# Kernel tuning notes

Measured on AMD Instinct MI355X. Metric: run time of the kernel, lower is better.

The kernel has to match this reference:

```python
import jax, jax.numpy as jnp
import numpy as np

D_MODEL = 1024
N_HEADS = 16
HEAD_DIM = D_MODEL // N_HEADS


def setup_inputs() -> dict:
    key = jax.random.key(0)
    ks = jax.random.split(key, 5)
    x = jax.random.normal(ks[0], (2, 2048, D_MODEL), dtype=jnp.float32)
    s = 1.0 / np.sqrt(D_MODEL)
    W_qkv = jax.random.normal(ks[1], (D_MODEL, 3 * D_MODEL), dtype=jnp.float32) * s
    b_qkv = jnp.zeros((3 * D_MODEL,), dtype=jnp.float32)
    W_proj = jax.random.normal(ks[2], (D_MODEL, D_MODEL), dtype=jnp.float32) * s
    b_proj = jnp.zeros((D_MODEL,), dtype=jnp.float32)
    return {"x": x, "W_qkv": W_qkv, "b_qkv": b_qkv, "W_proj": W_proj, "b_proj": b_proj}


def reference(x, W_qkv, b_qkv, W_proj, b_proj):
    b, t, c = x.shape
    qkv = x @ W_qkv + b_qkv  # [b,t,3c]
    q, k, v = jnp.split(qkv, 3, axis=-1)
    # [b, h, t, d]
    q = q.reshape(b, t, N_HEADS, HEAD_DIM).transpose(0, 2, 1, 3)
    k = k.reshape(b, t, N_HEADS, HEAD_DIM).transpose(0, 2, 1, 3)
    v = v.reshape(b, t, N_HEADS, HEAD_DIM).transpose(0, 2, 1, 3)
    att = jnp.einsum('bhqd,bhkd->bhqk', q, k) / np.sqrt(HEAD_DIM)
    causal = jnp.tril(jnp.ones((t, t), dtype=bool))  # [t,t]
    att = jnp.where(causal[None, None], att, -jnp.inf)
    att = jax.nn.softmax(att, axis=-1)
    out = jnp.einsum('bhqk,bhkd->bhqd', att, v)  # [b,h,t,d]
    out = out.transpose(0, 2, 1, 3).reshape(b, t, c)
    return out @ W_proj + b_proj
```

## Files before the change

kernel.cpp:

```cpp
#include <hip/hip_runtime.h>
#include <hip/hip_bf16.h>

#define NB 2
#define NH 16
#define HD 64
#define DM 1024
#define TT 2048

typedef __attribute__((ext_vector_type(4))) float f32x4;
typedef __attribute__((ext_vector_type(8))) short bf16x8;

__device__ __forceinline__ unsigned short f2bf(float f) {
  union { float f; unsigned int i; } x; x.f = f;
  unsigned int r = x.i + 0x7fffu + ((x.i >> 16) & 1u);
  return (unsigned short)(r >> 16);
}

__device__ __forceinline__ void async16(unsigned short* lds_base, const unsigned short* g) {
  __builtin_amdgcn_global_load_lds(
      (const __attribute__((address_space(1))) void*)g,
      (__attribute__((address_space(3))) void*)lds_base, 16, 0, 0);
}

__global__ __launch_bounds__(256)
void convert_bf16_kernel(const float* __restrict__ in, unsigned short* __restrict__ out, int n8)
{
  const int i = blockIdx.x * 256 + threadIdx.x;
  if (i >= n8) return;
  const f32x4 a = *(const f32x4*)(in + (size_t)i * 8);
  const f32x4 b = *(const f32x4*)(in + (size_t)i * 8 + 4);
  uint4 o;
  o.x = f2bf(a.x) | ((unsigned)f2bf(a.y) << 16);
  o.y = f2bf(a.z) | ((unsigned)f2bf(a.w) << 16);
  o.z = f2bf(b.x) | ((unsigned)f2bf(b.y) << 16);
  o.w = f2bf(b.z) | ((unsigned)f2bf(b.w) << 16);
  *(uint4*)(out + (size_t)i * 8) = o;
}

__global__ __launch_bounds__(256)
void transpose_convert(const float* __restrict__ W, unsigned short* __restrict__ WT,
                       int K, int N)
{
  __shared__ unsigned short T[64][72];
  const int t = threadIdx.x;
  const int k0 = blockIdx.y * 64, n0 = blockIdx.x * 64;
  const int r = t >> 2;
  const int c = (t & 3) * 16;
  const float* src = W + (size_t)(k0 + r) * N + n0 + c;
  #pragma unroll
  for (int s = 0; s < 4; ++s) {
    const f32x4 v = *(const f32x4*)(src + s * 4);
    T[c + s*4 + 0][r] = f2bf(v.x);
    T[c + s*4 + 1][r] = f2bf(v.y);
    T[c + s*4 + 2][r] = f2bf(v.z);
    T[c + s*4 + 3][r] = f2bf(v.w);
  }
  __syncthreads();
  unsigned short* dst = WT + (size_t)(n0 + r) * K + k0 + c;
  *(uint4*)(dst)     = *(const uint4*)(&T[r][c]);
  *(uint4*)(dst + 8) = *(const uint4*)(&T[r][c + 8]);
}

template<int MODE>
__global__ __launch_bounds__(256)
void gemm_bf16(const unsigned short* __restrict__ A, const unsigned short* __restrict__ BT,
               const float* __restrict__ bias, void* __restrict__ Cout,
               int M, int N, int K)
{
  __shared__ unsigned short As[128 * 32];
  __shared__ unsigned short Bs[128 * 32];
  const int tid = threadIdx.x;
  const int lane = tid & 63;
  const int w = tid >> 6;
  const int wr = w >> 1, wc = w & 1;
  const int l15 = lane & 15, g = lane >> 4;
  const int m0 = blockIdx.y * 128;
  const int n0 = blockIdx.x * 128;

  f32x4 acc[4][4] = {};

  const int ar0 = tid >> 2,          as0 = (tid & 3) * 8;
  const int ar1 = (256 + tid) >> 2;
  const unsigned short* A0 = A + (size_t)(m0 + ar0) * K + as0;
  const unsigned short* A1 = A + (size_t)(m0 + ar1) * K + as0;
  const unsigned short* B0 = BT + (size_t)(n0 + ar0) * K + as0;
  const unsigned short* B1 = BT + (size_t)(n0 + ar1) * K + as0;
  unsigned short* AsW0 = &As[(0 * 256 + w * 64) * 8];
  unsigned short* AsW1 = &As[(1 * 256 + w * 64) * 8];
  unsigned short* BsW0 = &Bs[(0 * 256 + w * 64) * 8];
  unsigned short* BsW1 = &Bs[(1 * 256 + w * 64) * 8];

  for (int k0 = 0; k0 < K; k0 += 32) {
    async16(AsW0, A0 + k0);
    async16(AsW1, A1 + k0);
    async16(BsW0, B0 + k0);
    async16(BsW1, B1 + k0);
    __syncthreads();

    bf16x8 af[4], bfv[4];
    #pragma unroll
    for (int i = 0; i < 4; ++i)
      af[i] = *(const bf16x8*)(&As[(wr * 64 + i * 16 + l15) * 32 + g * 8]);
    #pragma unroll
    for (int j = 0; j < 4; ++j)
      bfv[j] = *(const bf16x8*)(&Bs[(wc * 64 + j * 16 + l15) * 32 + g * 8]);
    #pragma unroll
    for (int i = 0; i < 4; ++i)
      #pragma unroll
      for (int j = 0; j < 4; ++j)
        acc[i][j] = __builtin_amdgcn_mfma_f32_16x16x32_bf16(af[i], bfv[j], acc[i][j], 0, 0, 0);
    __syncthreads();
  }

  #pragma unroll
  for (int i = 0; i < 4; ++i) {
    #pragma unroll
    for (int j = 0; j < 4; ++j) {
      #pragma unroll
      for (int e = 0; e < 4; ++e) {
        const int row = m0 + wr * 64 + i * 16 + g * 4 + e;
        const int col = n0 + wc * 64 + j * 16 + l15;
        float val = acc[i][j][e] + bias[col];
        if (MODE == 0) {
          const int which = col >> 10;
          if (which == 0) val *= 0.125f;
          const int rem = col & 1023;
          const int hh = rem >> 6, dd = rem & 63;
          const int bb = row >> 11, tt = row & 2047;
          ((unsigned short*)Cout)[((((size_t)which * NB + bb) * NH + hh) * TT + tt) * HD + dd] = f2bf(val);
        } else {
          ((float*)Cout)[(size_t)row * N + col] = val;
        }
      }
    }
  }
}

__global__ __launch_bounds__(256)
void attn_kernel(const unsigned short* __restrict__ qkv, unsigned short* __restrict__ attn_out)
{
  __shared__ unsigned short Ksm[64 * 72];
  __shared__ unsigned short VTsm[64 * 72];
  __shared__ unsigned short Psm[4][32 * 72];

  const int tid = threadIdx.x;
  const int lane = tid & 63;
  const int wv = tid >> 6;
  const int l15 = lane & 15;
  const int g = lane >> 4;
  const int ip = blockIdx.x;
  const int bh = blockIdx.y;
  const int qlo0 = ip * 64;
  const int qhi0 = (31 - ip) * 64;

  const size_t base = (size_t)bh * TT * HD;
  const unsigned short* Qg = qkv + base;
  const unsigned short* Kg = qkv + (size_t)NB * NH * TT * HD + base;
  const unsigned short* Vg = qkv + (size_t)2 * NB * NH * TT * HD + base;

  const int qr_lo = qlo0 + wv * 16 + l15;
  const int qr_hi = qhi0 + wv * 16 + l15;
  const bf16x8 qlf0 = *(const bf16x8*)(Qg + (size_t)qr_lo * HD + g * 8);
  const bf16x8 qlf1 = *(const bf16x8*)(Qg + (size_t)qr_lo * HD + 32 + g * 8);
  const bf16x8 qhf0 = *(const bf16x8*)(Qg + (size_t)qr_hi * HD + g * 8);
  const bf16x8 qhf1 = *(const bf16x8*)(Qg + (size_t)qr_hi * HD + 32 + g * 8);

  f32x4 olo[4] = {}, ohi[4] = {};
  float llo[4] = {0.f, 0.f, 0.f, 0.f};
  float lhi[4] = {0.f, 0.f, 0.f, 0.f};

  const int krow = tid >> 2;
  const int kseg = (tid & 3) * 16;
  const int vr0 = (tid >> 4) * 4;
  const int vc0 = (tid & 15) * 4;

  const int nt = 32 - ip;

  uint4 kra, krb;
  uint2 vreg[4];
  {
    const unsigned short* kp = Kg + (size_t)krow * HD + kseg;
    kra = *(const uint4*)(kp);
    krb = *(const uint4*)(kp + 8);
    #pragma unroll
    for (int i = 0; i < 4; ++i)
      vreg[i] = *(const uint2*)(Vg + (size_t)(vr0 + i) * HD + vc0);
  }

  for (int t = 0; t < nt; ++t) {
    const int t0 = t * 64;
    const bool lo_act = (t <= ip);
    __syncthreads();
    *(uint4*)(&Ksm[krow * 72 + kseg])     = kra;
    *(uint4*)(&Ksm[krow * 72 + kseg + 8]) = krb;
    {
      unsigned short a[4][4];
      #pragma unroll
      for (int i = 0; i < 4; ++i) {
        a[i][0] = (unsigned short)(vreg[i].x & 0xffffu);
        a[i][1] = (unsigned short)(vreg[i].x >> 16);
        a[i][2] = (unsigned short)(vreg[i].y & 0xffffu);
        a[i][3] = (unsigned short)(vreg[i].y >> 16);
      }
      #pragma unroll
      for (int j = 0; j < 4; ++j) {
        ushort4 col;
        col.x = a[0][j]; col.y = a[1][j]; col.z = a[2][j]; col.w = a[3][j];
        *(ushort4*)(&VTsm[(vc0 + j) * 72 + vr0]) = col;
      }
    }
    __syncthreads();

    if (t + 1 < nt) {
      const int t1 = t0 + 64;
      const unsigned short* kp = Kg + (size_t)(t1 + krow) * HD + kseg;
      kra = *(const uint4*)(kp);
      krb = *(const uint4*)(kp + 8);
      #pragma unroll
      for (int i = 0; i < 4; ++i)
        vreg[i] = *(const uint2*)(Vg + (size_t)(t1 + vr0 + i) * HD + vc0);
    }

    f32x4 slo[4] = {}, shi[4] = {};
    __builtin_amdgcn_s_setprio(1);
    #pragma unroll
    for (int j = 0; j < 4; ++j) {
      const bf16x8 kf0 = *(const bf16x8*)(&Ksm[(j * 16 + l15) * 72 + g * 8]);
      const bf16x8 kf1 = *(const bf16x8*)(&Ksm[(j * 16 + l15) * 72 + 32 + g * 8]);
      shi[j] = __builtin_amdgcn_mfma_f32_16x16x32_bf16(qhf0, kf0, shi[j], 0, 0, 0);
      shi[j] = __builtin_amdgcn_mfma_f32_16x16x32_bf16(qhf1, kf1, shi[j], 0, 0, 0);
      if (lo_act) {
        slo[j] = __builtin_amdgcn_mfma_f32_16x16x32_bf16(qlf0, kf0, slo[j], 0, 0, 0);
        slo[j] = __builtin_amdgcn_mfma_f32_16x16x32_bf16(qlf1, kf1, slo[j], 0, 0, 0);
      }
    }
    __builtin_amdgcn_s_setprio(0);
    if (t == nt - 1) {
      #pragma unroll
      for (int j = 0; j < 4; ++j)
        #pragma unroll
        for (int e = 0; e < 4; ++e)
          if (t0 + j * 16 + l15 > qhi0 + wv * 16 + 4 * g + e) shi[j][e] = -INFINITY;
    }
    if (t == ip) {
      #pragma unroll
      for (int j = 0; j < 4; ++j)
        #pragma unroll
        for (int e = 0; e < 4; ++e)
          if (t0 + j * 16 + l15 > qlo0 + wv * 16 + 4 * g + e) slo[j][e] = -INFINITY;
    }

    #pragma unroll
    for (int e = 0; e < 4; ++e) {
      const float p0 = __expf(shi[0][e]);
      const float p1 = __expf(shi[1][e]);
      const float p2 = __expf(shi[2][e]);
      const float p3 = __expf(shi[3][e]);
      lhi[e] += (p0 + p1) + (p2 + p3);
      unsigned short* pr = &Psm[wv][(16 + 4 * g + e) * 72];
      pr[l15]      = f2bf(p0);
      pr[16 + l15] = f2bf(p1);
      pr[32 + l15] = f2bf(p2);
      pr[48 + l15] = f2bf(p3);
    }
    if (lo_act) {
      #pragma unroll
      for (int e = 0; e < 4; ++e) {
        const float p0 = __expf(slo[0][e]);
        const float p1 = __expf(slo[1][e]);
        const float p2 = __expf(slo[2][e]);
        const float p3 = __expf(slo[3][e]);
        llo[e] += (p0 + p1) + (p2 + p3);
        unsigned short* pr = &Psm[wv][(4 * g + e) * 72];
        pr[l15]      = f2bf(p0);
        pr[16 + l15] = f2bf(p1);
        pr[32 + l15] = f2bf(p2);
        pr[48 + l15] = f2bf(p3);
      }
    }

    __builtin_amdgcn_s_setprio(1);
    #pragma unroll
    for (int c = 0; c < 2; ++c) {
      const bf16x8 pfh = *(const bf16x8*)(&Psm[wv][(16 + l15) * 72 + c * 32 + g * 8]);
      bf16x8 pfl;
      if (lo_act) pfl = *(const bf16x8*)(&Psm[wv][l15 * 72 + c * 32 + g * 8]);
      #pragma unroll
      for (int db = 0; db < 4; ++db) {
        const bf16x8 vf = *(const bf16x8*)(&VTsm[(db * 16 + l15) * 72 + c * 32 + g * 8]);
        ohi[db] = __builtin_amdgcn_mfma_f32_16x16x32_bf16(pfh, vf, ohi[db], 0, 0, 0);
        if (lo_act) olo[db] = __builtin_amdgcn_mfma_f32_16x16x32_bf16(pfl, vf, olo[db], 0, 0, 0);
      }
    }
    __builtin_amdgcn_s_setprio(0);
  }

  #pragma unroll
  for (int e = 0; e < 4; ++e) {
    #pragma unroll
    for (int off = 1; off < 16; off <<= 1) {
      llo[e] += __shfl_xor(llo[e], off, 64);
      lhi[e] += __shfl_xor(lhi[e], off, 64);
    }
  }

  const int bb = bh >> 4;
  const int hh = bh & 15;
  #pragma unroll
  for (int e = 0; e < 4; ++e) {
    const float invl = 1.f / llo[e];
    const float invh = 1.f / lhi[e];
    const int ql = qlo0 + wv * 16 + 4 * g + e;
    const int qh = qhi0 + wv * 16 + 4 * g + e;
    #pragma unroll
    for (int db = 0; db < 4; ++db) {
      attn_out[(size_t)(bb * TT + ql) * DM + hh * HD + db * 16 + l15] = f2bf(olo[db][e] * invl);
      attn_out[(size_t)(bb * TT + qh) * DM + hh * HD + db * 16 + l15] = f2bf(ohi[db][e] * invh);
    }
  }
}

extern "C" void kernel_launch(void* const* d_in, const int* in_sizes, int n_in,
                              void* d_out, int out_size, void* d_ws, size_t ws_size,
                              hipStream_t stream)
{
  const float* x     = (const float*)d_in[0];
  const float* Wqkv  = (const float*)d_in[1];
  const float* bqkv  = (const float*)d_in[2];
  const float* Wproj = (const float*)d_in[3];
  const float* bproj = (const float*)d_in[4];

  const size_t qkv_elems = (size_t)3 * NB * NH * TT * HD;
  unsigned short* qkv_ws  = (unsigned short*)d_ws;
  unsigned short* WqkvT   = qkv_ws + qkv_elems;
  unsigned short* WprojT  = WqkvT + (size_t)3 * DM * DM;
  unsigned short* xbf     = WprojT + (size_t)DM * DM;
  unsigned short* attn_ws = xbf;

  dim3 blk(256, 1, 1);
  hipLaunchKernelGGL(convert_bf16_kernel, dim3((NB * TT * DM / 8 + 255) / 256, 1, 1), blk, 0, stream,
                     x, xbf, NB * TT * DM / 8);
  hipLaunchKernelGGL(transpose_convert, dim3(3 * DM / 64, DM / 64, 1), blk, 0, stream,
                     Wqkv, WqkvT, DM, 3 * DM);
  hipLaunchKernelGGL(transpose_convert, dim3(DM / 64, DM / 64, 1), blk, 0, stream,
                     Wproj, WprojT, DM, DM);
  hipLaunchKernelGGL((gemm_bf16<0>), dim3(3 * DM / 128, NB * TT / 128, 1), blk, 0, stream,
                     xbf, WqkvT, bqkv, (void*)qkv_ws, NB * TT, 3 * DM, DM);
  hipLaunchKernelGGL(attn_kernel, dim3(16, NB * NH, 1), blk, 0, stream,
                     qkv_ws, attn_ws);
  hipLaunchKernelGGL((gemm_bf16<1>), dim3(DM / 128, NB * TT / 128, 1), blk, 0, stream,
                     attn_ws, WprojT, bproj, d_out, NB * TT, DM, DM);
}
```

Measured before the change: 145.7 us.

## Split attention into smaller 2-wave blocks with XCD-aware mapping and transposed scores

Result: slower. 173.1 us (+18.8%).

```diff
diff --git a/kernel.cpp b/kernel.cpp
--- a/kernel.cpp
+++ b/kernel.cpp
@@ -14,6 +14,12 @@
   union { float f; unsigned int i; } x; x.f = f;
   unsigned int r = x.i + 0x7fffu + ((x.i >> 16) & 1u);
   return (unsigned short)(r >> 16);
+}
+
+__device__ __forceinline__ unsigned int cvtpk(float lo, float hi) {
+  unsigned int r;
+  asm("v_cvt_pk_bf16_f32 %0, %1, %2" : "=v"(r) : "v"(lo), "v"(hi));
+  return r;
 }
 
 __device__ __forceinline__ void async16(unsigned short* lds_base, const unsigned short* g) {
@@ -136,22 +142,27 @@
   }
 }
 
-__global__ __launch_bounds__(256)
+__global__ __launch_bounds__(128)
 void attn_kernel(const unsigned short* __restrict__ qkv, unsigned short* __restrict__ attn_out)
 {
   __shared__ unsigned short Ksm[64 * 72];
   __shared__ unsigned short VTsm[64 * 72];
-  __shared__ unsigned short Psm[4][32 * 72];
+  __shared__ unsigned short Psm[2][32 * 72];
 
   const int tid = threadIdx.x;
   const int lane = tid & 63;
   const int wv = tid >> 6;
   const int l15 = lane & 15;
   const int g = lane >> 4;
-  const int ip = blockIdx.x;
-  const int bh = blockIdx.y;
-  const int qlo0 = ip * 64;
-  const int qhi0 = (31 - ip) * 64;
+
+  const int li = blockIdx.x + gridDim.x * blockIdx.y;
+  const int xcd = li & 7;
+  const int tt_ = li >> 3;
+  const int ip = tt_ & 31;
+  const int bh = ((tt_ >> 5) << 3) | xcd;
+
+  const int qlo0 = ip * 32;
+  const int qhi0 = (63 - ip) * 32;
 
   const size_t base = (size_t)bh * TT * HD;
   const unsigned short* Qg = qkv + base;
@@ -166,116 +177,119 @@
   const bf16x8 qhf1 = *(const bf16x8*)(Qg + (size_t)qr_hi * HD + 32 + g * 8);
 
   f32x4 olo[4] = {}, ohi[4] = {};
-  float llo[4] = {0.f, 0.f, 0.f, 0.f};
-  float lhi[4] = {0.f, 0.f, 0.f, 0.f};
-
-  const int krow = tid >> 2;
-  const int kseg = (tid & 3) * 16;
+  float llo = 0.f, lhi = 0.f;
+
+  const int krow = tid >> 1;
+  const int kcol = (tid & 1) * 32;
   const int vr0 = (tid >> 4) * 4;
   const int vc0 = (tid & 15) * 4;
 
-  const int nt = 32 - ip;
-
-  uint4 kra, krb;
-  uint2 vreg[4];
+  const int nt    = ((63 - ip) >> 1) + 1;
+  const int lo_nt = (ip >> 1) + 1;
+
+  uint4 kr[4];
+  uint2 vreg[2][4];
   {
-    const unsigned short* kp = Kg + (size_t)krow * HD + kseg;
-    kra = *(const uint4*)(kp);
-    krb = *(const uint4*)(kp + 8);
-    #pragma unroll
-    for (int i = 0; i < 4; ++i)
-      vreg[i] = *(const uint2*)(Vg + (size_t)(vr0 + i) * HD + vc0);
+    const unsigned short* kp = Kg + (size_t)krow * HD + kcol;
+    #pragma unroll
+    for (int j = 0; j < 4; ++j) kr[j] = *(const uint4*)(kp + j * 8);
+    #pragma unroll
+    for (int m = 0; m < 2; ++m)
+      #pragma unroll
+      for (int r = 0; r < 4; ++r)
+        vreg[m][r] = *(const uint2*)(Vg + (size_t)(vr0 + 32 * m + r) * HD + vc0);
   }
 
   for (int t = 0; t < nt; ++t) {
     const int t0 = t * 64;
-    const bool lo_act = (t <= ip);
+    const bool lo_act = (t < lo_nt);
     __syncthreads();
-    *(uint4*)(&Ksm[krow * 72 + kseg])     = kra;
-    *(uint4*)(&Ksm[krow * 72 + kseg + 8]) = krb;
-    {
+    #pragma unroll
+    for (int j = 0; j < 4; ++j)
+      *(uint4*)(&Ksm[krow * 72 + kcol + j * 8]) = kr[j];
+    #pragma unroll
+    for (int m = 0; m < 2; ++m) {
       unsigned short a[4][4];
       #pragma unroll
       for (int i = 0; i < 4; ++i) {
-        a[i][0] = (unsigned short)(vreg[i].x & 0xffffu);
-        a[i][1] = (unsigned short)(vreg[i].x >> 16);
-        a[i][2] = (unsigned short)(vreg[i].y & 0xffffu);
-        a[i][3] = (unsigned short)(vreg[i].y >> 16);
-      }
-      #pragma unroll
-      for (int j = 0; j < 4; ++j) {
+        a[i][0] = (unsigned short)(vreg[m][i].x & 0xffffu);
+        a[i][1] = (unsigned short)(vreg[m][i].x >> 16);
+        a[i][2] = (unsigned short)(vreg[m][i].y & 0xffffu);
+        a[i][3] = (unsigned short)(vreg[m][i].y >> 16);
+      }
+      #pragma unroll
+      for (int c = 0; c < 4; ++c) {
         ushort4 col;
-        col.x = a[0][j]; col.y = a[1][j]; col.z = a[2][j]; col.w = a[3][j];
-        *(ushort4*)(&VTsm[(vc0 + j) * 72 + vr0]) = col;
+        col.x = a[0][c]; col.y = a[1][c]; col.z = a[2][c]; col.w = a[3][c];
+        *(ushort4*)(&VTsm[(vc0 + c) * 72 + vr0 + 32 * m]) = col;
       }
     }
     __syncthreads();
 
     if (t + 1 < nt) {
       const int t1 = t0 + 64;
-      const unsigned short* kp = Kg + (size_t)(t1 + krow) * HD + kseg;
-      kra = *(const uint4*)(kp);
-      krb = *(const uint4*)(kp + 8);
-      #pragma unroll
-      for (int i = 0; i < 4; ++i)
-        vreg[i] = *(const uint2*)(Vg + (size_t)(t1 + vr0 + i) * HD + vc0);
-    }
-
-    f32x4 slo[4] = {}, shi[4] = {};
+      const unsigned short* kp = Kg + (size_t)(t1 + krow) * HD + kcol;
+      #pragma unroll
+      for (int j = 0; j < 4; ++j) kr[j] = *(const uint4*)(kp + j * 8);
+      #pragma unroll
+      for (int m = 0; m < 2; ++m)
+        #pragma unroll
+        for (int r = 0; r < 4; ++r)
+          vreg[m][r] = *(const uint2*)(Vg + (size_t)(t1 + vr0 + 32 * m + r) * HD + vc0);
+    }
+
+    f32x4 shiT[4] = {}, sloT[4] = {};
     __builtin_amdgcn_s_setprio(1);
     #pragma unroll
-    for (int j = 0; j < 4; ++j) {
-      const bf16x8 kf0 = *(const bf16x8*)(&Ksm[(j * 16 + l15) * 72 + g * 8]);
-      const bf16x8 kf1 = *(const bf16x8*)(&Ksm[(j * 16 + l15) * 72 + 32 + g * 8]);
-      shi[j] = __builtin_amdgcn_mfma_f32_16x16x32_bf16(qhf0, kf0, shi[j], 0, 0, 0);
-      shi[j] = __builtin_amdgcn_mfma_f32_16x16x32_bf16(qhf1, kf1, shi[j], 0, 0, 0);
+    for (int b = 0; b < 4; ++b) {
+      const bf16x8 kf0 = *(const bf16x8*)(&Ksm[(b * 16 + l15) * 72 + g * 8]);
+      const bf16x8 kf1 = *(const bf16x8*)(&Ksm[(b * 16 + l15) * 72 + 32 + g * 8]);
+      shiT[b] = __builtin_amdgcn_mfma_f32_16x16x32_bf16(kf0, qhf0, shiT[b], 0, 0, 0);
+      shiT[b] = __builtin_amdgcn_mfma_f32_16x16x32_bf16(kf1, qhf1, shiT[b], 0, 0, 0);
       if (lo_act) {
-        slo[j] = __builtin_amdgcn_mfma_f32_16x16x32_bf16(qlf0, kf0, slo[j], 0, 0, 0);
-        slo[j] = __builtin_amdgcn_mfma_f32_16x16x32_bf16(qlf1, kf1, slo[j], 0, 0, 0);
+        sloT[b] = __builtin_amdgcn_mfma_f32_16x16x32_bf16(kf0, qlf0, sloT[b], 0, 0, 0);
+        sloT[b] = __builtin_amdgcn_mfma_f32_16x16x32_bf16(kf1, qlf1, sloT[b], 0, 0, 0);
       }
     }
     __builtin_amdgcn_s_setprio(0);
+
     if (t == nt - 1) {
-      #pragma unroll
-      for (int j = 0; j < 4; ++j)
+      const int qh = qhi0 + wv * 16 + l15;
+      #pragma unroll
+      for (int b = 0; b < 4; ++b)
         #pragma unroll
         for (int e = 0; e < 4; ++e)
-          if (t0 + j * 16 + l15 > qhi0 + wv * 16 + 4 * g + e) shi[j][e] = -INFINITY;
-    }
-    if (t == ip) {
-      #pragma unroll
-      for (int j = 0; j < 4; ++j)
+          if (t0 + b * 16 + 4 * g + e > qh) shiT[b][e] = -INFINITY;
+    }
+    if (lo_act && t == lo_nt - 1) {
+      const int ql = qlo0 + wv * 16 + l15;
+      #pragma unroll
+      for (int b = 0; b < 4; ++b)
         #pragma unroll
         for (int e = 0; e < 4; ++e)
-          if (t0 + j * 16 + l15 > qlo0 + wv * 16 + 4 * g + e) slo[j][e] = -INFINITY;
-    }
-
-    #pragma unroll
-    for (int e = 0; e < 4; ++e) {
-      const float p0 = __expf(shi[0][e]);
-      const float p1 = __expf(shi[1][e]);
-      const float p2 = __expf(shi[2][e]);
-      const float p3 = __expf(shi[3][e]);
-      lhi[e] += (p0 + p1) + (p2 + p3);
-      unsigned short* pr = &Psm[wv][(16 + 4 * g + e) * 72];
-      pr[l15]      = f2bf(p0);
-      pr[16 + l15] = f2bf(p1);
-      pr[32 + l15] = f2bf(p2);
-      pr[48 + l15] = f2bf(p3);
+          if (t0 + b * 16 + 4 * g + e > ql) sloT[b][e] = -INFINITY;
+    }
+
+    #pragma unroll
+    for (int b = 0; b < 4; ++b) {
+      const float p0 = __expf(shiT[b][0]);
+      const float p1 = __expf(shiT[b][1]);
+      const float p2 = __expf(shiT[b][2]);
+      const float p3 = __expf(shiT[b][3]);
+      lhi += (p0 + p1) + (p2 + p3);
+      uint2 wd; wd.x = cvtpk(p0, p1); wd.y = cvtpk(p2, p3);
+      *(uint2*)(&Psm[wv][(16 + l15) * 72 + b * 16 + 4 * g]) = wd;
     }
     if (lo_act) {
       #pragma unroll
-      for (int e = 0; e < 4; ++e) {
-        const float p0 = __expf(slo[0][e]);
-        const float p1 = __expf(slo[1][e]);
-        const float p2 = __expf(slo[2][e]);
-        const float p3 = __expf(slo[3][e]);
-        llo[e] += (p0 + p1) + (p2 + p3);
-        unsigned short* pr = &Psm[wv][(4 * g + e) * 72];
-        pr[l15]      = f2bf(p0);
-        pr[16 + l15] = f2bf(p1);
-        pr[32 + l15] = f2bf(p2);
-        pr[48 + l15] = f2bf(p3);
+      for (int b = 0; b < 4; ++b) {
+        const float p0 = __expf(sloT[b][0]);
+        const float p1 = __expf(sloT[b][1]);
+        const float p2 = __expf(sloT[b][2]);
+        const float p3 = __expf(sloT[b][3]);
+        llo += (p0 + p1) + (p2 + p3);
+        uint2 wd; wd.x = cvtpk(p0, p1); wd.y = cvtpk(p2, p3);
+        *(uint2*)(&Psm[wv][l15 * 72 + b * 16 + 4 * g]) = wd;
       }
     }
 
@@ -295,27 +309,23 @@
     __builtin_amdgcn_s_setprio(0);
   }
 
-  #pragma unroll
-  for (int e = 0; e < 4; ++e) {
-    #pragma unroll
-    for (int off = 1; off < 16; off <<= 1) {
-      llo[e] += __shfl_xor(llo[e], off, 64);
-      lhi[e] += __shfl_xor(lhi[e], off, 64);
-    }
-  }
+  lhi += __shfl_xor(lhi, 16, 64);
+  lhi += __shfl_xor(lhi, 32, 64);
+  llo += __shfl_xor(llo, 16, 64);
+  llo += __shfl_xor(llo, 32, 64);
 
   const int bb = bh >> 4;
   const int hh = bh & 15;
   #pragma unroll
   for (int e = 0; e < 4; ++e) {
-    const float invl = 1.f / llo[e];
-    const float invh = 1.f / lhi[e];
+    const float invh = 1.f / __shfl(lhi, 4 * g + e, 64);
+    const float invl = 1.f / __shfl(llo, 4 * g + e, 64);
+    const int qh = qhi0 + wv * 16 + 4 * g + e;
     const int ql = qlo0 + wv * 16 + 4 * g + e;
-    const int qh = qhi0 + wv * 16 + 4 * g + e;
     #pragma unroll
     for (int db = 0; db < 4; ++db) {
+      attn_out[(size_t)(bb * TT + qh) * DM + hh * HD + db * 16 + l15] = f2bf(ohi[db][e] * invh);
       attn_out[(size_t)(bb * TT + ql) * DM + hh * HD + db * 16 + l15] = f2bf(olo[db][e] * invl);
-      attn_out[(size_t)(bb * TT + qh) * DM + hh * HD + db * 16 + l15] = f2bf(ohi[db][e] * invh);
     }
   }
 }
@@ -337,17 +347,16 @@
   unsigned short* xbf     = WprojT + (size_t)DM * DM;
   unsigned short* attn_ws = xbf;
 
-  dim3 blk(256, 1, 1);
-  hipLaunchKernelGGL(convert_bf16_kernel, dim3((NB * TT * DM / 8 + 255) / 256, 1, 1), blk, 0, stream,
+  hipLaunchKernelGGL(convert_bf16_kernel, dim3((NB * TT * DM / 8 + 255) / 256, 1, 1), dim3(256), 0, stream,
                      x, xbf, NB * TT * DM / 8);
-  hipLaunchKernelGGL(transpose_convert, dim3(3 * DM / 64, DM / 64, 1), blk, 0, stream,
+  hipLaunchKernelGGL(transpose_convert, dim3(3 * DM / 64, DM / 64, 1), dim3(256), 0, stream,
                      Wqkv, WqkvT, DM, 3 * DM);
-  hipLaunchKernelGGL(transpose_convert, dim3(DM / 64, DM / 64, 1), blk, 0, stream,
+  hipLaunchKernelGGL(transpose_convert, dim3(DM / 64, DM / 64, 1), dim3(256), 0, stream,
                      Wproj, WprojT, DM, DM);
-  hipLaunchKernelGGL((gemm_bf16<0>), dim3(3 * DM / 128, NB * TT / 128, 1), blk, 0, stream,
+  hipLaunchKernelGGL((gemm_bf16<0>), dim3(3 * DM / 128, NB * TT / 128, 1), dim3(256), 0, stream,
                      xbf, WqkvT, bqkv, (void*)qkv_ws, NB * TT, 3 * DM, DM);
-  hipLaunchKernelGGL(attn_kernel, dim3(16, NB * NH, 1), blk, 0, stream,
+  hipLaunchKernelGGL(attn_kernel, dim3(32, 32, 1), dim3(128), 0, stream,
                      qkv_ws, attn_ws);
-  hipLaunchKernelGGL((gemm_bf16<1>), dim3(DM / 128, NB * TT / 128, 1), blk, 0, stream,
+  hipLaunchKernelGGL((gemm_bf16<1>), dim3(DM / 128, NB * TT / 128, 1), dim3(256), 0, stream,
                      attn_ws, WprojT, bproj, d_out, NB * TT, DM, DM);
 }
```
